# Optimization experiments

Measured on AMD Instinct MI355X. Metric: run time of the kernel, lower is better.

Reference implementation:

```python
import jax, jax.numpy as jnp
import numpy as np

N_NODES = 10000
N_EDGES = 640000
D_IN, D_HID, D_OUT = 128, 128, 64


def setup_inputs() -> dict:
    key = jax.random.key(0)
    ks = jax.random.split(key, 12)
    inp = {
        "inputs": jax.random.normal(ks[0], (N_NODES, D_IN), dtype=jnp.float32),
        "W_self0": jax.random.normal(ks[1], (D_IN, D_HID), dtype=jnp.float32) / np.sqrt(D_IN),
        "W_neigh0": jax.random.normal(ks[2], (D_IN, D_HID), dtype=jnp.float32) / np.sqrt(D_IN),
        "b0": jnp.zeros((D_HID,), dtype=jnp.float32),
        "W_self1": jax.random.normal(ks[3], (D_HID, D_HID), dtype=jnp.float32) / np.sqrt(D_HID),
        "W_neigh1": jax.random.normal(ks[4], (D_HID, D_HID), dtype=jnp.float32) / np.sqrt(D_HID),
        "b1": jnp.zeros((D_HID,), dtype=jnp.float32),
        "W_self2": jax.random.normal(ks[5], (D_HID, D_OUT), dtype=jnp.float32) / np.sqrt(D_HID),
        "W_neigh2": jax.random.normal(ks[6], (D_HID, D_OUT), dtype=jnp.float32) / np.sqrt(D_HID),
        "b2": jnp.zeros((D_OUT,), dtype=jnp.float32),
        "edge_src": jax.random.randint(ks[7], (N_EDGES,), 0, N_NODES, dtype=jnp.int32),
        "edge_dst": jax.random.randint(ks[8], (N_EDGES,), 0, N_NODES, dtype=jnp.int32),
    }
    return inp


def _sage_conv(h, W_self, W_neigh, b, edge_src, edge_dst):
    # mean aggregation: mean of source-node features over incoming edges at dst
    gathered = h[edge_src]                                   # [E, d] irregular gather
    agg = jax.ops.segment_sum(gathered, edge_dst, num_segments=N_NODES)  # [N, d]
    deg = jax.ops.segment_sum(jnp.ones((edge_dst.shape[0],), h.dtype), edge_dst,
                              num_segments=N_NODES)          # [N]
    h_neigh = agg / jnp.maximum(deg, 1.0)[:, None]
    return h @ W_self + h_neigh @ W_neigh + b


def reference(inputs, W_self0, W_neigh0, b0, W_self1, W_neigh1, b1,
              W_self2, W_neigh2, b2, edge_src, edge_dst):
    # dropout p=0.0 -> identity
    h = _sage_conv(inputs, W_self0, W_neigh0, b0, edge_src, edge_dst)
    h = jax.nn.relu(h)
    h = _sage_conv(h, W_self1, W_neigh1, b1, edge_src, edge_dst)
    h = jax.nn.relu(h)
    h = _sage_conv(h, W_self2, W_neigh2, b2, edge_src, edge_dst)
    return h
```

## Files before the change

kernel.cpp:

```cpp
#include <hip/hip_runtime.h>


#define NN 10000
#define NE 640000
#define NBINS 313
#define NBLKA 250
#define CHUNK 2560
#define CAP 3072
#define SORT_CAP 4096

typedef __attribute__((ext_vector_type(8))) short s8v;
typedef __attribute__((ext_vector_type(4))) float f4v;

__device__ __forceinline__ ushort f2bf(float f) {
    unsigned u = __float_as_uint(f);
    return (ushort)((u + 0x7FFFu + ((u >> 16) & 1u)) >> 16);
}
__device__ __forceinline__ unsigned pack2(float a, float b) {
    return (unsigned)f2bf(a) | ((unsigned)f2bf(b) << 16);
}
__device__ __forceinline__ float bf_lo(unsigned u) { return __uint_as_float(u << 16); }
__device__ __forceinline__ float bf_hi(unsigned u) { return __uint_as_float(u & 0xFFFF0000u); }

__device__ void wtrans_body(const float* __restrict__ W, ushort* __restrict__ dst,
                            int MC, ushort* ps) {
    int tid = threadIdx.x;
    int tot = 128 * MC;
    for (int idx = tid; idx < tot; idx += 256) {
        int k = (MC == 128) ? (idx >> 7) : (idx >> 6);
        int n = (MC == 128) ? (idx & 127) : (idx & 63);
        ps[n * 128 + k] = f2bf(W[idx]);
    }
    __syncthreads();
    for (int idx = tid; idx < tot; idx += 256)
        dst[idx] = ps[idx];
}


__global__ void prep_k(const float* __restrict__ Ws0, const float* __restrict__ Wn0,
                       ushort* __restrict__ wt, int* __restrict__ bincnt) {
    __shared__ ushort ps[128 * 128];
    int blk = blockIdx.x, tid = threadIdx.x;
    if (blk == 0) {
        for (int i = tid; i < NBINS; i += 256) bincnt[i] = 0;
        wtrans_body(Ws0, wt, 128, ps);
    } else {
        wtrans_body(Wn0, wt + 16384, 128, ps);
    }
}


__device__ void scatter_body(const int* __restrict__ src, const int* __restrict__ dst,
                             int* __restrict__ bincnt, unsigned* __restrict__ tmp2,
                             int blk, int* smem) {
    int* h = smem;
    int* cur = smem + NBINS;
    unsigned* ec = (unsigned*)(smem + 2 * NBINS);
    int tid = threadIdx.x;
    for (int i = tid; i < NBINS; i += 256) h[i] = 0;
    __syncthreads();
    int base = blk * CHUNK;
    for (int i = tid; i < CHUNK; i += 256) {
        int d = dst[base + i], s = src[base + i];
        int bin = d >> 5;
        ec[i] = ((unsigned)bin << 19) | ((unsigned)s << 5) | (unsigned)(d & 31);
        atomicAdd(&h[bin], 1);
    }
    __syncthreads();
    for (int bin = tid; bin < NBINS; bin += 256) {
        int c = h[bin];
        int off = c ? atomicAdd(&bincnt[bin], c) : 0;
        cur[bin] = bin * CAP + off;
    }
    __syncthreads();
    for (int i = tid; i < CHUNK; i += 256) {
        unsigned word = ec[i];
        int bin = (int)(word >> 19);
        int pos = atomicAdd(&cur[bin], 1);
        if (pos < bin * CAP + CAP)
            tmp2[pos] = word & 0x7FFFFu;
    }
}

__device__ void dense0_body(const float* __restrict__ x, const ushort* __restrict__ wt,
                            const float* __restrict__ b0,
                            float* __restrict__ hs, ushort* __restrict__ hn, int dblk) {
    int l = threadIdx.x & 63, w = threadIdx.x >> 6;
    int mloc = l & 15, quad = l >> 4;
    int row_base = dblk * 32 + (w & 1) * 16;
    int colh = w >> 1;
    int arow = row_base + mloc;
    int arow_c = (arow < NN) ? arow : (NN - 1);
    const float4* xrow = (const float4*)(x + (size_t)arow_c * 128);
    const ushort* wsT = wt;
    const ushort* wnT = wt + 16384;
    f4v accS[4], accN[4];
#pragma unroll
    for (int nt = 0; nt < 4; ++nt) { accS[nt] = (f4v){0,0,0,0}; accN[nt] = (f4v){0,0,0,0}; }
#pragma unroll
    for (int ks = 0; ks < 4; ++ks) {
        int kb = ks * 32 + quad * 8;
        float4 f0 = xrow[kb >> 2];
        float4 f1 = xrow[(kb >> 2) + 1];
        s8v a;
        a[0] = (short)f2bf(f0.x); a[1] = (short)f2bf(f0.y);
        a[2] = (short)f2bf(f0.z); a[3] = (short)f2bf(f0.w);
        a[4] = (short)f2bf(f1.x); a[5] = (short)f2bf(f1.y);
        a[6] = (short)f2bf(f1.z); a[7] = (short)f2bf(f1.w);
#pragma unroll
        for (int nt = 0; nt < 4; ++nt) {
            int n = colh * 64 + nt * 16 + mloc;
            s8v bs = *(const s8v*)(wsT + n * 128 + kb);
            s8v bn = *(const s8v*)(wnT + n * 128 + kb);
            accS[nt] = __builtin_amdgcn_mfma_f32_16x16x32_bf16(a, bs, accS[nt], 0, 0, 0);
            accN[nt] = __builtin_amdgcn_mfma_f32_16x16x32_bf16(a, bn, accN[nt], 0, 0, 0);
        }
    }
#pragma unroll
    for (int nt = 0; nt < 4; ++nt) {
        int col = colh * 64 + nt * 16 + mloc;
        float bv = b0[col];
#pragma unroll
        for (int r = 0; r < 4; ++r) {
            int row = row_base + quad * 4 + r;
            if (row < NN) {
                hs[(size_t)row * 128 + col] = accS[nt][r] + bv;
                hn[(size_t)row * 128 + col] = f2bf(accN[nt][r]);
            }
        }
    }
}

__global__ void scatdense_k(const int* __restrict__ esrc, const int* __restrict__ edst,
                            int* __restrict__ bincnt, unsigned* __restrict__ tmp2,
                            const float* __restrict__ x, ushort* __restrict__ wt,
                            const float* __restrict__ b0,
                            float* __restrict__ hs, ushort* __restrict__ hn,
                            const float* __restrict__ Ws1, const float* __restrict__ Wn1,
                            const float* __restrict__ Ws2, const float* __restrict__ Wn2) {
    __shared__ ushort ps[128 * 128];
    int blk = blockIdx.x;
    if (blk < NBLKA) {
        scatter_body(esrc, edst, bincnt, tmp2, blk, (int*)ps);
    } else if (blk < NBLKA + 313) {
        dense0_body(x, wt, b0, hs, hn, blk - NBLKA);
    } else {
        int m = blk - NBLKA - 313;
        const float* W = (m == 0) ? Ws1 : (m == 1) ? Wn1 : (m == 2) ? Ws2 : Wn2;
        int MC = (m < 2) ? 128 : 64;
        ushort* dst = wt + ((m < 2) ? 32768 + m * 16384 : 65536 + (m - 2) * 8192);
        wtrans_body(W, dst, MC, ps);
    }
}


__global__ void sort_k(const unsigned* __restrict__ tmp2, const int* __restrict__ bincnt,
                       int* __restrict__ offs, int* __restrict__ ends,
                       int* __restrict__ ssrc) {
    __shared__ int stage[SORT_CAP];
    __shared__ int cnt32[32];
    __shared__ int cur32[32];
    int b = blockIdx.x, tid = threadIdx.x;
    int beg = b * CAP;
    int cnt = bincnt[b];
    if (cnt > CAP) cnt = CAP;
    if (tid < 32) cnt32[tid] = 0;
    __syncthreads();
    for (int i = tid; i < cnt; i += 256)
        atomicAdd(&cnt32[tmp2[beg + i] & 31], 1);
    __syncthreads();
    if (tid == 0) {
        int run = 0;
        for (int i = 0; i < 32; ++i) {
            int node = b * 32 + i;
            if (node < NN) { offs[node] = beg + run; ends[node] = beg + run + cnt32[i]; }
            cur32[i] = run;
            run += cnt32[i];
        }
    }
    __syncthreads();
    for (int i = tid; i < cnt; i += 256) {
        unsigned q = tmp2[beg + i];
        int pos = atomicAdd(&cur32[q & 31], 1);
        stage[pos] = (int)(q >> 5);
    }
    __syncthreads();
    for (int i = tid; i < cnt; i += 256)
        ssrc[beg + i] = stage[i];
}


template <int MOUT>
__global__ void agg_dense_k(const float* __restrict__ hs_in, const ushort* __restrict__ hn_in,
                            const int* __restrict__ offs, const int* __restrict__ ends,
                            const int* __restrict__ ssrc,
                            const ushort* __restrict__ wsT, const ushort* __restrict__ wnT,
                            const float* __restrict__ bias,
                            float* __restrict__ hs_out, ushort* __restrict__ hn_out) {
    __shared__ ushort hrow[16 * 136];
    int tid = threadIdx.x;
    int node_loc = tid >> 4, t = tid & 15;
    int node = blockIdx.x * 16 + node_loc;
    int beg = offs[node], end = ends[node];
    const uint4* hn4 = (const uint4*)hn_in;
    float a0 = 0, a1 = 0, a2 = 0, a3 = 0, a4 = 0, a5 = 0, a6 = 0, a7 = 0;
    int e = beg;
    for (; e + 8 <= end; e += 8) {
        int s0 = ssrc[e], s1 = ssrc[e + 1], s2 = ssrc[e + 2], s3 = ssrc[e + 3];
        int s4 = ssrc[e + 4], s5 = ssrc[e + 5], s6 = ssrc[e + 6], s7 = ssrc[e + 7];
        uint4 v0 = hn4[(size_t)s0 * 16 + t];
        uint4 v1 = hn4[(size_t)s1 * 16 + t];
        uint4 v2 = hn4[(size_t)s2 * 16 + t];
        uint4 v3 = hn4[(size_t)s3 * 16 + t];
        uint4 v4 = hn4[(size_t)s4 * 16 + t];
        uint4 v5 = hn4[(size_t)s5 * 16 + t];
        uint4 v6 = hn4[(size_t)s6 * 16 + t];
        uint4 v7 = hn4[(size_t)s7 * 16 + t];
        a0 += bf_lo(v0.x) + bf_lo(v1.x) + bf_lo(v2.x) + bf_lo(v3.x)
            + bf_lo(v4.x) + bf_lo(v5.x) + bf_lo(v6.x) + bf_lo(v7.x);
        a1 += bf_hi(v0.x) + bf_hi(v1.x) + bf_hi(v2.x) + bf_hi(v3.x)
            + bf_hi(v4.x) + bf_hi(v5.x) + bf_hi(v6.x) + bf_hi(v7.x);
        a2 += bf_lo(v0.y) + bf_lo(v1.y) + bf_lo(v2.y) + bf_lo(v3.y)
            + bf_lo(v4.y) + bf_lo(v5.y) + bf_lo(v6.y) + bf_lo(v7.y);
        a3 += bf_hi(v0.y) + bf_hi(v1.y) + bf_hi(v2.y) + bf_hi(v3.y)
            + bf_hi(v4.y) + bf_hi(v5.y) + bf_hi(v6.y) + bf_hi(v7.y);
        a4 += bf_lo(v0.z) + bf_lo(v1.z) + bf_lo(v2.z) + bf_lo(v3.z)
            + bf_lo(v4.z) + bf_lo(v5.z) + bf_lo(v6.z) + bf_lo(v7.z);
        a5 += bf_hi(v0.z) + bf_hi(v1.z) + bf_hi(v2.z) + bf_hi(v3.z)
            + bf_hi(v4.z) + bf_hi(v5.z) + bf_hi(v6.z) + bf_hi(v7.z);
        a6 += bf_lo(v0.w) + bf_lo(v1.w) + bf_lo(v2.w) + bf_lo(v3.w)
            + bf_lo(v4.w) + bf_lo(v5.w) + bf_lo(v6.w) + bf_lo(v7.w);
        a7 += bf_hi(v0.w) + bf_hi(v1.w) + bf_hi(v2.w) + bf_hi(v3.w)
            + bf_hi(v4.w) + bf_hi(v5.w) + bf_hi(v6.w) + bf_hi(v7.w);
    }
    for (; e < end; ++e) {
        uint4 v = hn4[(size_t)ssrc[e] * 16 + t];
        a0 += bf_lo(v.x); a1 += bf_hi(v.x); a2 += bf_lo(v.y); a3 += bf_hi(v.y);
        a4 += bf_lo(v.z); a5 += bf_hi(v.z); a6 += bf_lo(v.w); a7 += bf_hi(v.w);
    }
    int deg = end - beg;
    float sc = 1.0f / (float)(deg > 0 ? deg : 1);
    float4 h4a = ((const float4*)hs_in)[(size_t)node * 32 + 2 * t];
    float4 h4b = ((const float4*)hs_in)[(size_t)node * 32 + 2 * t + 1];
    float r0 = fmaxf(h4a.x + a0 * sc, 0.f), r1 = fmaxf(h4a.y + a1 * sc, 0.f);
    float r2 = fmaxf(h4a.z + a2 * sc, 0.f), r3 = fmaxf(h4a.w + a3 * sc, 0.f);
    float r4 = fmaxf(h4b.x + a4 * sc, 0.f), r5 = fmaxf(h4b.y + a5 * sc, 0.f);
    float r6 = fmaxf(h4b.z + a6 * sc, 0.f), r7 = fmaxf(h4b.w + a7 * sc, 0.f);
    *(uint4*)(hrow + node_loc * 136 + t * 8) =
        make_uint4(pack2(r0, r1), pack2(r2, r3), pack2(r4, r5), pack2(r6, r7));
    __syncthreads();

    int l = tid & 63, w = tid >> 6;
    int mloc = l & 15, quad = l >> 4;
    constexpr int NTPW = MOUT / 64;
    f4v accS[NTPW], accN[NTPW];
#pragma unroll
    for (int nt = 0; nt < NTPW; ++nt) { accS[nt] = (f4v){0,0,0,0}; accN[nt] = (f4v){0,0,0,0}; }
#pragma unroll
    for (int ks = 0; ks < 4; ++ks) {
        int kb = ks * 32 + quad * 8;
        s8v a = *(const s8v*)(hrow + mloc * 136 + kb);
#pragma unroll
        for (int nt = 0; nt < NTPW; ++nt) {
            int n = (w * NTPW + nt) * 16 + mloc;
            s8v bs = *(const s8v*)(wsT + n * 128 + kb);
            s8v bn = *(const s8v*)(wnT + n * 128 + kb);
            accS[nt] = __builtin_amdgcn_mfma_f32_16x16x32_bf16(a, bs, accS[nt], 0, 0, 0);
            accN[nt] = __builtin_amdgcn_mfma_f32_16x16x32_bf16(a, bn, accN[nt], 0, 0, 0);
        }
    }
#pragma unroll
    for (int nt = 0; nt < NTPW; ++nt) {
        int col = (w * NTPW + nt) * 16 + mloc;
        float bv = bias[col];
#pragma unroll
        for (int r = 0; r < 4; ++r) {
            int row = blockIdx.x * 16 + quad * 4 + r;
            hs_out[(size_t)row * MOUT + col] = accS[nt][r] + bv;
            hn_out[(size_t)row * MOUT + col] = f2bf(accN[nt][r]);
        }
    }
}


__global__ void agg_out_k(const float* __restrict__ hs_in, const ushort* __restrict__ hn_in,
                          const int* __restrict__ offs, const int* __restrict__ ends,
                          const int* __restrict__ ssrc, float* __restrict__ out) {
    int tid = threadIdx.x;
    int node = blockIdx.x * 32 + (tid >> 3);
    int t = tid & 7;
    if (node >= NN) return;
    int beg = offs[node], end = ends[node];
    const uint4* hn4 = (const uint4*)hn_in;
    float a0 = 0, a1 = 0, a2 = 0, a3 = 0, a4 = 0, a5 = 0, a6 = 0, a7 = 0;
    int e = beg;
    for (; e + 8 <= end; e += 8) {
        int s0 = ssrc[e], s1 = ssrc[e + 1], s2 = ssrc[e + 2], s3 = ssrc[e + 3];
        int s4 = ssrc[e + 4], s5 = ssrc[e + 5], s6 = ssrc[e + 6], s7 = ssrc[e + 7];
        uint4 v0 = hn4[(size_t)s0 * 8 + t];
        uint4 v1 = hn4[(size_t)s1 * 8 + t];
        uint4 v2 = hn4[(size_t)s2 * 8 + t];
        uint4 v3 = hn4[(size_t)s3 * 8 + t];
        uint4 v4 = hn4[(size_t)s4 * 8 + t];
        uint4 v5 = hn4[(size_t)s5 * 8 + t];
        uint4 v6 = hn4[(size_t)s6 * 8 + t];
        uint4 v7 = hn4[(size_t)s7 * 8 + t];
        a0 += bf_lo(v0.x) + bf_lo(v1.x) + bf_lo(v2.x) + bf_lo(v3.x)
            + bf_lo(v4.x) + bf_lo(v5.x) + bf_lo(v6.x) + bf_lo(v7.x);
        a1 += bf_hi(v0.x) + bf_hi(v1.x) + bf_hi(v2.x) + bf_hi(v3.x)
            + bf_hi(v4.x) + bf_hi(v5.x) + bf_hi(v6.x) + bf_hi(v7.x);
        a2 += bf_lo(v0.y) + bf_lo(v1.y) + bf_lo(v2.y) + bf_lo(v3.y)
            + bf_lo(v4.y) + bf_lo(v5.y) + bf_lo(v6.y) + bf_lo(v7.y);
        a3 += bf_hi(v0.y) + bf_hi(v1.y) + bf_hi(v2.y) + bf_hi(v3.y)
            + bf_hi(v4.y) + bf_hi(v5.y) + bf_hi(v6.y) + bf_hi(v7.y);
        a4 += bf_lo(v0.z) + bf_lo(v1.z) + bf_lo(v2.z) + bf_lo(v3.z)
            + bf_lo(v4.z) + bf_lo(v5.z) + bf_lo(v6.z) + bf_lo(v7.z);
        a5 += bf_hi(v0.z) + bf_hi(v1.z) + bf_hi(v2.z) + bf_hi(v3.z)
            + bf_hi(v4.z) + bf_hi(v5.z) + bf_hi(v6.z) + bf_hi(v7.z);
        a6 += bf_lo(v0.w) + bf_lo(v1.w) + bf_lo(v2.w) + bf_lo(v3.w)
            + bf_lo(v4.w) + bf_lo(v5.w) + bf_lo(v6.w) + bf_lo(v7.w);
        a7 += bf_hi(v0.w) + bf_hi(v1.w) + bf_hi(v2.w) + bf_hi(v3.w)
            + bf_hi(v4.w) + bf_hi(v5.w) + bf_hi(v6.w) + bf_hi(v7.w);
    }
    for (; e < end; ++e) {
        uint4 v = hn4[(size_t)ssrc[e] * 8 + t];
        a0 += bf_lo(v.x); a1 += bf_hi(v.x); a2 += bf_lo(v.y); a3 += bf_hi(v.y);
        a4 += bf_lo(v.z); a5 += bf_hi(v.z); a6 += bf_lo(v.w); a7 += bf_hi(v.w);
    }
    int deg = end - beg;
    float sc = 1.0f / (float)(deg > 0 ? deg : 1);
    float4 h4a = ((const float4*)hs_in)[(size_t)node * 16 + 2 * t];
    float4 h4b = ((const float4*)hs_in)[(size_t)node * 16 + 2 * t + 1];
    ((float4*)out)[(size_t)node * 16 + 2 * t] =
        make_float4(h4a.x + a0 * sc, h4a.y + a1 * sc, h4a.z + a2 * sc, h4a.w + a3 * sc);
    ((float4*)out)[(size_t)node * 16 + 2 * t + 1] =
        make_float4(h4b.x + a4 * sc, h4b.y + a5 * sc, h4b.z + a6 * sc, h4b.w + a7 * sc);
}


extern "C" void kernel_launch(void* const* d_in, const int* in_sizes, int n_in,
                              void* d_out, int out_size, void* d_ws, size_t ws_size,
                              hipStream_t stream) {
    const float* x   = (const float*)d_in[0];
    const float* Ws0 = (const float*)d_in[1];
    const float* Wn0 = (const float*)d_in[2];
    const float* b0  = (const float*)d_in[3];
    const float* Ws1 = (const float*)d_in[4];
    const float* Wn1 = (const float*)d_in[5];
    const float* b1  = (const float*)d_in[6];
    const float* Ws2 = (const float*)d_in[7];
    const float* Wn2 = (const float*)d_in[8];
    const float* b2  = (const float*)d_in[9];
    const int* esrc  = (const int*)d_in[10];
    const int* edst  = (const int*)d_in[11];
    float* out = (float*)d_out;

    float*  hsA = (float*)d_ws;
    float*  hsB = hsA + (size_t)NN * 128;
    ushort* hnA = (ushort*)(hsB + (size_t)NN * 128);
    ushort* hnB = hnA + (size_t)NN * 128;
    ushort* wt  = hnB + (size_t)NN * 128;
    unsigned* tmp2 = (unsigned*)(wt + 81920);
    int* ssrc = (int*)(tmp2 + (size_t)NBINS * CAP);
    int* offs = ssrc + (size_t)NBINS * CAP;
    int* ends = offs + NN;
    int* bincnt = ends + NN;

    prep_k<<<2, 256, 0, stream>>>(Ws0, Wn0, wt, bincnt);
    scatdense_k<<<NBLKA + 313 + 4, 256, 0, stream>>>(esrc, edst, bincnt, tmp2,
                                                     x, wt, b0, hsA, hnA,
                                                     Ws1, Wn1, Ws2, Wn2);
    sort_k<<<NBINS, 256, 0, stream>>>(tmp2, bincnt, offs, ends, ssrc);
    agg_dense_k<128><<<NN / 16, 256, 0, stream>>>(hsA, hnA, offs, ends, ssrc,
                                                  wt + 32768, wt + 49152, b1, hsB, hnB);
    agg_dense_k<64><<<NN / 16, 256, 0, stream>>>(hsB, hnB, offs, ends, ssrc,
                                                 wt + 65536, wt + 73728, b2, hsA, hnA);
    agg_out_k<<<(NN + 31) / 32, 256, 0, stream>>>(hsA, hnA, offs, ends, ssrc, out);
}
```

Baseline: 166.5 us.

## Replace binned edge sort with direct per-node atomic slot scatter

Drops the two-stage bin scatter plus the separate sort kernel. Each edge now takes a slot in a fixed 128-entry row per destination node through a global atomic counter, and the aggregation kernels read the per-node count directly. This removes one kernel launch and an extra pass over the edge list. The neighbour-index loads in the aggregation loops also become int4 vector loads. In exchange it adds contention on global atomics and a larger, sparser index buffer. Edges beyond 128 per node are silently dropped, and the edge order within a node is no longer deterministic.

```diff
diff --git a/kernel.cpp b/kernel.cpp
--- a/kernel.cpp
+++ b/kernel.cpp
@@ -3,11 +3,9 @@
 
 #define NN 10000
 #define NE 640000
-#define NBINS 313
-#define NBLKA 250
-#define CHUNK 2560
-#define CAP 3072
-#define SORT_CAP 4096
+#define NBLKS 256
+#define EPB 2500
+#define CAPN 128
 
 typedef __attribute__((ext_vector_type(8))) short s8v;
 typedef __attribute__((ext_vector_type(4))) float f4v;
@@ -38,11 +36,11 @@
 
 
 __global__ void prep_k(const float* __restrict__ Ws0, const float* __restrict__ Wn0,
-                       ushort* __restrict__ wt, int* __restrict__ bincnt) {
+                       ushort* __restrict__ wt, int* __restrict__ cnt) {
     __shared__ ushort ps[128 * 128];
     int blk = blockIdx.x, tid = threadIdx.x;
+    for (int i = tid; i < NN / 2; i += 256) cnt[blk * (NN / 2) + i] = 0;
     if (blk == 0) {
-        for (int i = tid; i < NBINS; i += 256) bincnt[i] = 0;
         wtrans_body(Ws0, wt, 128, ps);
     } else {
         wtrans_body(Wn0, wt + 16384, 128, ps);
@@ -51,34 +49,14 @@
 
 
 __device__ void scatter_body(const int* __restrict__ src, const int* __restrict__ dst,
-                             int* __restrict__ bincnt, unsigned* __restrict__ tmp2,
-                             int blk, int* smem) {
-    int* h = smem;
-    int* cur = smem + NBINS;
-    unsigned* ec = (unsigned*)(smem + 2 * NBINS);
+                             int* __restrict__ cnt, int* __restrict__ ssrc, int blk) {
     int tid = threadIdx.x;
-    for (int i = tid; i < NBINS; i += 256) h[i] = 0;
-    __syncthreads();
-    int base = blk * CHUNK;
-    for (int i = tid; i < CHUNK; i += 256) {
+    int base = blk * EPB;
+    for (int i = tid; i < EPB; i += 256) {
         int d = dst[base + i], s = src[base + i];
-        int bin = d >> 5;
-        ec[i] = ((unsigned)bin << 19) | ((unsigned)s << 5) | (unsigned)(d & 31);
-        atomicAdd(&h[bin], 1);
-    }
-    __syncthreads();
-    for (int bin = tid; bin < NBINS; bin += 256) {
-        int c = h[bin];
-        int off = c ? atomicAdd(&bincnt[bin], c) : 0;
-        cur[bin] = bin * CAP + off;
-    }
-    __syncthreads();
-    for (int i = tid; i < CHUNK; i += 256) {
-        unsigned word = ec[i];
-        int bin = (int)(word >> 19);
-        int pos = atomicAdd(&cur[bin], 1);
-        if (pos < bin * CAP + CAP)
-            tmp2[pos] = word & 0x7FFFFu;
+        int pos = atomicAdd(&cnt[d], 1);
+        if (pos < CAPN)
+            ssrc[(d << 7) + pos] = s;
     }
 }
 
@@ -132,7 +110,7 @@
 }
 
 __global__ void scatdense_k(const int* __restrict__ esrc, const int* __restrict__ edst,
-                            int* __restrict__ bincnt, unsigned* __restrict__ tmp2,
+                            int* __restrict__ cnt, int* __restrict__ ssrc,
                             const float* __restrict__ x, ushort* __restrict__ wt,
                             const float* __restrict__ b0,
                             float* __restrict__ hs, ushort* __restrict__ hn,
@@ -140,12 +118,12 @@
                             const float* __restrict__ Ws2, const float* __restrict__ Wn2) {
     __shared__ ushort ps[128 * 128];
     int blk = blockIdx.x;
-    if (blk < NBLKA) {
-        scatter_body(esrc, edst, bincnt, tmp2, blk, (int*)ps);
-    } else if (blk < NBLKA + 313) {
-        dense0_body(x, wt, b0, hs, hn, blk - NBLKA);
+    if (blk < NBLKS) {
+        scatter_body(esrc, edst, cnt, ssrc, blk);
+    } else if (blk < NBLKS + 313) {
+        dense0_body(x, wt, b0, hs, hn, blk - NBLKS);
     } else {
-        int m = blk - NBLKA - 313;
+        int m = blk - NBLKS - 313;
         const float* W = (m == 0) ? Ws1 : (m == 1) ? Wn1 : (m == 2) ? Ws2 : Wn2;
         int MC = (m < 2) ? 128 : 64;
         ushort* dst = wt + ((m < 2) ? 32768 + m * 16384 : 65536 + (m - 2) * 8192);
@@ -154,46 +132,9 @@
 }
 
 
-__global__ void sort_k(const unsigned* __restrict__ tmp2, const int* __restrict__ bincnt,
-                       int* __restrict__ offs, int* __restrict__ ends,
-                       int* __restrict__ ssrc) {
-    __shared__ int stage[SORT_CAP];
-    __shared__ int cnt32[32];
-    __shared__ int cur32[32];
-    int b = blockIdx.x, tid = threadIdx.x;
-    int beg = b * CAP;
-    int cnt = bincnt[b];
-    if (cnt > CAP) cnt = CAP;
-    if (tid < 32) cnt32[tid] = 0;
-    __syncthreads();
-    for (int i = tid; i < cnt; i += 256)
-        atomicAdd(&cnt32[tmp2[beg + i] & 31], 1);
-    __syncthreads();
-    if (tid == 0) {
-        int run = 0;
-        for (int i = 0; i < 32; ++i) {
-            int node = b * 32 + i;
-            if (node < NN) { offs[node] = beg + run; ends[node] = beg + run + cnt32[i]; }
-            cur32[i] = run;
-            run += cnt32[i];
-        }
-    }
-    __syncthreads();
-    for (int i = tid; i < cnt; i += 256) {
-        unsigned q = tmp2[beg + i];
-        int pos = atomicAdd(&cur32[q & 31], 1);
-        stage[pos] = (int)(q >> 5);
-    }
-    __syncthreads();
-    for (int i = tid; i < cnt; i += 256)
-        ssrc[beg + i] = stage[i];
-}
-
-
 template <int MOUT>
 __global__ void agg_dense_k(const float* __restrict__ hs_in, const ushort* __restrict__ hn_in,
-                            const int* __restrict__ offs, const int* __restrict__ ends,
-                            const int* __restrict__ ssrc,
+                            const int* __restrict__ cnt, const int* __restrict__ ssrc,
                             const ushort* __restrict__ wsT, const ushort* __restrict__ wnT,
                             const float* __restrict__ bias,
                             float* __restrict__ hs_out, ushort* __restrict__ hn_out) {
@@ -201,21 +142,23 @@
     int tid = threadIdx.x;
     int node_loc = tid >> 4, t = tid & 15;
     int node = blockIdx.x * 16 + node_loc;
-    int beg = offs[node], end = ends[node];
+    int deg = cnt[node];
+    if (deg > CAPN) deg = CAPN;
+    int beg = node << 7, end = beg + deg;
     const uint4* hn4 = (const uint4*)hn_in;
     float a0 = 0, a1 = 0, a2 = 0, a3 = 0, a4 = 0, a5 = 0, a6 = 0, a7 = 0;
     int e = beg;
     for (; e + 8 <= end; e += 8) {
-        int s0 = ssrc[e], s1 = ssrc[e + 1], s2 = ssrc[e + 2], s3 = ssrc[e + 3];
-        int s4 = ssrc[e + 4], s5 = ssrc[e + 5], s6 = ssrc[e + 6], s7 = ssrc[e + 7];
-        uint4 v0 = hn4[(size_t)s0 * 16 + t];
-        uint4 v1 = hn4[(size_t)s1 * 16 + t];
-        uint4 v2 = hn4[(size_t)s2 * 16 + t];
-        uint4 v3 = hn4[(size_t)s3 * 16 + t];
-        uint4 v4 = hn4[(size_t)s4 * 16 + t];
-        uint4 v5 = hn4[(size_t)s5 * 16 + t];
-        uint4 v6 = hn4[(size_t)s6 * 16 + t];
-        uint4 v7 = hn4[(size_t)s7 * 16 + t];
+        int4 sA = *(const int4*)(ssrc + e);
+        int4 sB = *(const int4*)(ssrc + e + 4);
+        uint4 v0 = hn4[(size_t)sA.x * 16 + t];
+        uint4 v1 = hn4[(size_t)sA.y * 16 + t];
+        uint4 v2 = hn4[(size_t)sA.z * 16 + t];
+        uint4 v3 = hn4[(size_t)sA.w * 16 + t];
+        uint4 v4 = hn4[(size_t)sB.x * 16 + t];
+        uint4 v5 = hn4[(size_t)sB.y * 16 + t];
+        uint4 v6 = hn4[(size_t)sB.z * 16 + t];
+        uint4 v7 = hn4[(size_t)sB.w * 16 + t];
         a0 += bf_lo(v0.x) + bf_lo(v1.x) + bf_lo(v2.x) + bf_lo(v3.x)
             + bf_lo(v4.x) + bf_lo(v5.x) + bf_lo(v6.x) + bf_lo(v7.x);
         a1 += bf_hi(v0.x) + bf_hi(v1.x) + bf_hi(v2.x) + bf_hi(v3.x)
@@ -238,7 +181,6 @@
         a0 += bf_lo(v.x); a1 += bf_hi(v.x); a2 += bf_lo(v.y); a3 += bf_hi(v.y);
         a4 += bf_lo(v.z); a5 += bf_hi(v.z); a6 += bf_lo(v.w); a7 += bf_hi(v.w);
     }
-    int deg = end - beg;
     float sc = 1.0f / (float)(deg > 0 ? deg : 1);
     float4 h4a = ((const float4*)hs_in)[(size_t)node * 32 + 2 * t];
     float4 h4b = ((const float4*)hs_in)[(size_t)node * 32 + 2 * t + 1];
@@ -284,27 +226,29 @@
 
 
 __global__ void agg_out_k(const float* __restrict__ hs_in, const ushort* __restrict__ hn_in,
-                          const int* __restrict__ offs, const int* __restrict__ ends,
-                          const int* __restrict__ ssrc, float* __restrict__ out) {
+                          const int* __restrict__ cnt, const int* __restrict__ ssrc,
+                          float* __restrict__ out) {
     int tid = threadIdx.x;
     int node = blockIdx.x * 32 + (tid >> 3);
     int t = tid & 7;
     if (node >= NN) return;
-    int beg = offs[node], end = ends[node];
+    int deg = cnt[node];
+    if (deg > CAPN) deg = CAPN;
+    int beg = node << 7, end = beg + deg;
     const uint4* hn4 = (const uint4*)hn_in;
     float a0 = 0, a1 = 0, a2 = 0, a3 = 0, a4 = 0, a5 = 0, a6 = 0, a7 = 0;
     int e = beg;
     for (; e + 8 <= end; e += 8) {
-        int s0 = ssrc[e], s1 = ssrc[e + 1], s2 = ssrc[e + 2], s3 = ssrc[e + 3];
-        int s4 = ssrc[e + 4], s5 = ssrc[e + 5], s6 = ssrc[e + 6], s7 = ssrc[e + 7];
-        uint4 v0 = hn4[(size_t)s0 * 8 + t];
-        uint4 v1 = hn4[(size_t)s1 * 8 + t];
-        uint4 v2 = hn4[(size_t)s2 * 8 + t];
-        uint4 v3 = hn4[(size_t)s3 * 8 + t];
-        uint4 v4 = hn4[(size_t)s4 * 8 + t];
-        uint4 v5 = hn4[(size_t)s5 * 8 + t];
-        uint4 v6 = hn4[(size_t)s6 * 8 + t];
-        uint4 v7 = hn4[(size_t)s7 * 8 + t];
+        int4 sA = *(const int4*)(ssrc + e);
+        int4 sB = *(const int4*)(ssrc + e + 4);
+        uint4 v0 = hn4[(size_t)sA.x * 8 + t];
+        uint4 v1 = hn4[(size_t)sA.y * 8 + t];
+        uint4 v2 = hn4[(size_t)sA.z * 8 + t];
+        uint4 v3 = hn4[(size_t)sA.w * 8 + t];
+        uint4 v4 = hn4[(size_t)sB.x * 8 + t];
+        uint4 v5 = hn4[(size_t)sB.y * 8 + t];
+        uint4 v6 = hn4[(size_t)sB.z * 8 + t];
+        uint4 v7 = hn4[(size_t)sB.w * 8 + t];
         a0 += bf_lo(v0.x) + bf_lo(v1.x) + bf_lo(v2.x) + bf_lo(v3.x)
             + bf_lo(v4.x) + bf_lo(v5.x) + bf_lo(v6.x) + bf_lo(v7.x);
         a1 += bf_hi(v0.x) + bf_hi(v1.x) + bf_hi(v2.x) + bf_hi(v3.x)
@@ -327,7 +271,6 @@
         a0 += bf_lo(v.x); a1 += bf_hi(v.x); a2 += bf_lo(v.y); a3 += bf_hi(v.y);
         a4 += bf_lo(v.z); a5 += bf_hi(v.z); a6 += bf_lo(v.w); a7 += bf_hi(v.w);
     }
-    int deg = end - beg;
     float sc = 1.0f / (float)(deg > 0 ? deg : 1);
     float4 h4a = ((const float4*)hs_in)[(size_t)node * 16 + 2 * t];
     float4 h4b = ((const float4*)hs_in)[(size_t)node * 16 + 2 * t + 1];
@@ -360,20 +303,16 @@
     ushort* hnA = (ushort*)(hsB + (size_t)NN * 128);
     ushort* hnB = hnA + (size_t)NN * 128;
     ushort* wt  = hnB + (size_t)NN * 128;
-    unsigned* tmp2 = (unsigned*)(wt + 81920);
-    int* ssrc = (int*)(tmp2 + (size_t)NBINS * CAP);
-    int* offs = ssrc + (size_t)NBINS * CAP;
-    int* ends = offs + NN;
-    int* bincnt = ends + NN;
-
-    prep_k<<<2, 256, 0, stream>>>(Ws0, Wn0, wt, bincnt);
-    scatdense_k<<<NBLKA + 313 + 4, 256, 0, stream>>>(esrc, edst, bincnt, tmp2,
+    int* ssrc = (int*)(wt + 81920);
+    int* cnt  = ssrc + (size_t)NN * CAPN;
+
+    prep_k<<<2, 256, 0, stream>>>(Ws0, Wn0, wt, cnt);
+    scatdense_k<<<NBLKS + 313 + 4, 256, 0, stream>>>(esrc, edst, cnt, ssrc,
                                                      x, wt, b0, hsA, hnA,
                                                      Ws1, Wn1, Ws2, Wn2);
-    sort_k<<<NBINS, 256, 0, stream>>>(tmp2, bincnt, offs, ends, ssrc);
-    agg_dense_k<128><<<NN / 16, 256, 0, stream>>>(hsA, hnA, offs, ends, ssrc,
+    agg_dense_k<128><<<NN / 16, 256, 0, stream>>>(hsA, hnA, cnt, ssrc,
                                                   wt + 32768, wt + 49152, b1, hsB, hnB);
-    agg_dense_k<64><<<NN / 16, 256, 0, stream>>>(hsB, hnB, offs, ends, ssrc,
+    agg_dense_k<64><<<NN / 16, 256, 0, stream>>>(hsB, hnB, cnt, ssrc,
                                                  wt + 65536, wt + 73728, b2, hsA, hnA);
-    agg_out_k<<<(NN + 31) / 32, 256, 0, stream>>>(hsA, hnA, offs, ends, ssrc, out);
-}
+    agg_out_k<<<(NN + 31) / 32, 256, 0, stream>>>(hsA, hnA, cnt, ssrc, out);
+}
```

Result: slower. 186.5 us (+12.0%).
